# Performance work log

Measured on AMD Instinct MI355X. Metric: run time of the kernel, lower is better.

## Reference

```python
import jax, jax.numpy as jnp
import numpy as np

STRIDE = 16
PRE_K = 600
POST_K = 100
NMS_T = 0.7


def _gen_anchors(base=16.0, ratios=(0.5, 1.0, 2.0), scales=(8.0, 16.0, 32.0)):
    a = []
    for s in scales:
        for r in ratios:
            w = base * s * (r ** 0.5)
            h = base * s / (r ** 0.5)
            a.append([-w / 2, -h / 2, w / 2, h / 2])
    return jnp.asarray(a, jnp.float32)  # [9,4]


def _conv(x, w, b, pad):
    y = jax.lax.conv_general_dilated(x, w, (1, 1), [(pad, pad), (pad, pad)],
                                     dimension_numbers=("NCHW", "OIHW", "NCHW"))
    return y + b[None, :, None, None]


def _decode(deltas, anchors):
    w = anchors[:, 2] - anchors[:, 0]
    h = anchors[:, 3] - anchors[:, 1]
    cx = anchors[:, 0] + 0.5 * w
    cy = anchors[:, 1] + 0.5 * h
    dx, dy, dw, dh = deltas[:, 0], deltas[:, 1], deltas[:, 2], deltas[:, 3]
    pcx = cx + dx * w
    pcy = cy + dy * h
    pw = w * jnp.exp(dw)
    ph = h * jnp.exp(dh)
    return jnp.stack([pcx - 0.5 * pw, pcy - 0.5 * ph,
                      pcx + 0.5 * pw, pcy + 0.5 * ph], axis=-1)


def _nms_keep(boxes, thresh):
    # boxes already sorted by score descending; returns bool keep mask [N]
    x1, y1, x2, y2 = boxes[:, 0], boxes[:, 1], boxes[:, 2], boxes[:, 3]
    area = (x2 - x1) * (y2 - y1)
    xx1 = jnp.maximum(x1[:, None], x1[None, :])
    yy1 = jnp.maximum(y1[:, None], y1[None, :])
    xx2 = jnp.minimum(x2[:, None], x2[None, :])
    yy2 = jnp.minimum(y2[:, None], y2[None, :])
    inter = jnp.maximum(xx2 - xx1, 0.0) * jnp.maximum(yy2 - yy1, 0.0)
    iou = inter / (area[:, None] + area[None, :] - inter)
    n = boxes.shape[0]
    idx = jnp.arange(n)

    def body(i, keep):
        suppress = keep[i] & (iou[i] > thresh) & (idx > i)
        return keep & ~suppress

    return jax.lax.fori_loop(0, n, body, jnp.ones((n,), bool))


def setup_inputs() -> dict:
    key = jax.random.key(0)
    ks = jax.random.split(key, 7)
    C_in, C_mid, A = 256, 256, 9
    feats = jax.random.normal(ks[0], (4, C_in, 128, 128), jnp.float32)
    conv_w = jax.random.normal(ks[1], (C_mid, C_in, 3, 3), jnp.float32) * 0.02
    conv_b = jnp.zeros((C_mid,), jnp.float32)
    cls_w = jax.random.normal(ks[2], (A, C_mid, 1, 1), jnp.float32) * 0.05
    cls_b = jnp.zeros((A,), jnp.float32)
    bbox_w = jax.random.normal(ks[3], (A * 4, C_mid, 1, 1), jnp.float32) * 0.02
    bbox_b = jnp.zeros((A * 4,), jnp.float32)
    return {"features": feats, "conv_w": conv_w, "conv_b": conv_b,
            "cls_w": cls_w, "cls_b": cls_b, "bbox_w": bbox_w, "bbox_b": bbox_b,
            "image_h": 2048, "image_w": 2048}


def reference(features, conv_w, conv_b, cls_w, cls_b, bbox_w, bbox_b, image_h, image_w):
    B, _, H, W = features.shape
    A = cls_w.shape[0]
    t = jax.nn.relu(_conv(features, conv_w, conv_b, 1))
    logits = _conv(t, cls_w, cls_b, 0)        # [B,A,H,W]
    bbox_deltas = _conv(t, bbox_w, bbox_b, 0)  # [B,4A,H,W]

    anchors = _gen_anchors()
    sx = jnp.arange(W, dtype=jnp.float32) * STRIDE
    sy = jnp.arange(H, dtype=jnp.float32) * STRIDE
    gy, gx = jnp.meshgrid(sy, sx, indexing="ij")
    shifts = jnp.stack([gx, gy, gx, gy], axis=2).reshape(-1, 4)  # [HW,4]
    anchors_all = (anchors[None, :, :] + shifts[:, None, :]).reshape(-1, 4)  # [HW*A,4]

    scores = jnp.transpose(logits, (0, 2, 3, 1)).reshape(B, -1)          # [B,HWA]
    deltas = jnp.transpose(bbox_deltas, (0, 2, 3, 1)).reshape(B, -1, 4)  # [B,HWA,4]

    img_w = jnp.float32(image_w)
    img_h = jnp.float32(image_h)

    def per_image(s, d):
        p = _decode(d, anchors_all)
        p = jnp.stack([jnp.clip(p[:, 0], 0.0, img_w),
                       jnp.clip(p[:, 1], 0.0, img_h),
                       jnp.clip(p[:, 2], 0.0, img_w),
                       jnp.clip(p[:, 3], 0.0, img_h)], axis=-1)
        _, topi = jax.lax.top_k(s, PRE_K)
        p = p[topi]                                # [PRE_K,4] sorted by score
        keep = _nms_keep(p, NMS_T)
        order = jnp.argsort(jnp.where(keep, 0, 1), stable=True)  # kept first, score order
        sel = order[:POST_K]
        valid = keep[sel]
        return p[sel] * valid[:, None].astype(p.dtype)  # zero-pad suppressed slots

    return jax.vmap(per_image)(scores, deltas)  # [B,POST_K,4]
```

## Files before the change

### kernel.cpp

```cpp
#include <hip/hip_runtime.h>
#include <cstdint>
#include <cstddef>

#define BB 4
#define CIN 256
#define HH 128
#define WW 128
#define NANCH (HH*WW*9)
#define PRE_K 600
#define POST_K 100
#define NMS_T 0.7f
#define CAND_CAP 2048

typedef _Float16 f16x8 __attribute__((ext_vector_type(8)));
typedef float    f32x4 __attribute__((ext_vector_type(4)));

#define WS_SCORES 0
#define WS_DELTAS (BB*NANCH)
#define WS_WHI    (WS_DELTAS + BB*NANCH*4)
#define WS_WLO    (WS_WHI + 9*256*128)
#define WS_HIST   (WS_WLO + 9*256*128)
#define WS_CCNT   (WS_HIST + 8192)
#define WS_CAND   (WS_CCNT + 16)
#define WS_PHI    (WS_CAND + 16384)
#define WS_PLANE_F 8388608
#define WS_PLO    (WS_PHI + WS_PLANE_F)
#define WS_ZERO   (WS_PLO + WS_PLANE_F)
#define WS_TOTAL_FULL (WS_ZERO + 16)
#define WS_TOTAL_MIN  WS_PHI

__device__ inline unsigned score_key(float f) {
    unsigned u = __float_as_uint(f);
    return (u & 0x80000000u) ? ~u : (u | 0x80000000u);
}

__global__ __launch_bounds__(256)
void prep_all(const float* __restrict__ feat, const float* __restrict__ convw,
              _Float16* __restrict__ pHi, _Float16* __restrict__ pLo,
              _Float16* __restrict__ whi, _Float16* __restrict__ wlo,
              float* __restrict__ zeroPg, unsigned* __restrict__ ghist,
              int prepBlocks)
{
    const int blk = blockIdx.x;
    if (blk < prepBlocks) {
        const int id = blk * 256 + threadIdx.x;
        if (blk == 0 && threadIdx.x < 16) zeroPg[threadIdx.x] = 0.f;
        const int gx = id & 127;
        const int gy = (id >> 7) & 127;
        const int ck = (id >> 14) & 7;
        const int b  = id >> 17;
        const int g  = (((gx + 1) >> 1) & 1) | (((gy + 1) & 1) << 1);
        const float* fb = feat + ((size_t)(b*256 + ck*32) << 14) + (gy << 7) + gx;
        f16x8 gh[4], gl[4];
        #pragma unroll
        for (int icg = 0; icg < 4; ++icg)
            #pragma unroll
            for (int k = 0; k < 8; ++k) {
                const float v = fb[(size_t)(icg*8 + k) << 14] * 16.f;
                const _Float16 h = (_Float16)v;
                gh[icg][k] = h;
                gl[icg][k] = (_Float16)(v - (float)h);
            }
        char* Hc = (char*)pHi + (size_t)id * 64;
        char* Lc = (char*)pLo + (size_t)id * 64;
        #pragma unroll
        for (int icg = 0; icg < 4; ++icg) {
            const int p = icg ^ g;
            *(f16x8*)(Hc + p*16) = gh[icg];
            *(f16x8*)(Lc + p*16) = gl[icg];
        }
    } else if (blk < prepBlocks + 256) {
        const int g = (blk - prepBlocks) * 256 + threadIdx.x;
        if (g >= 65536) return;
        const int oc = g >> 8, ic = g & 255;
        const int chunk = ic >> 5, icl = ic & 31;
        #pragma unroll
        for (int t = 0; t < 9; ++t) {
            const float v = convw[(size_t)g*9 + t] * 64.f;
            const _Float16 h = (_Float16)v;
            const _Float16 lo = (_Float16)(v - (float)h);
            const size_t o = (size_t)((t*8 + chunk)*256 + oc)*32 + icl;
            whi[o] = h;
            wlo[o] = lo;
        }
    } else {
        const int id = (blk - prepBlocks - 256) * 256 + threadIdx.x;
        if (id < 8208) ghist[id] = 0u;
    }
}

__global__ __launch_bounds__(512, 2)
void conv_mfma(const float* __restrict__ feat, const float* __restrict__ convb,
               const _Float16* __restrict__ whi, const _Float16* __restrict__ wlo,
               const float* __restrict__ clsw, const float* __restrict__ bboxw,
               const float* __restrict__ clsb, const float* __restrict__ bboxb,
               const _Float16* __restrict__ pHi, const _Float16* __restrict__ pLo,
               const float* __restrict__ zeroPg, unsigned* __restrict__ ghist,
               float* __restrict__ scores, float* __restrict__ deltas)
{
    __shared__ __align__(16) unsigned char smem[87040];
    float* sBias = (float*)(smem + 86016);

    const int bid = blockIdx.x;
    const int b  = bid >> 6;
    const int ty = (bid >> 3) & 7;
    const int tx = bid & 7;
    const int h0 = ty*16, c0 = tx*16;
    const int tid = threadIdx.x;
    const int w   = tid >> 6;
    const int wm  = w >> 1;
    const int wph = w & 1;
    const int l  = tid & 63;
    const int q  = l >> 4;
    const int c  = l & 15;

    const float* featb = feat + (size_t)b*CIN*HH*WW;
    const int wOff = (wm*64 + c)*32 + q*8;

    if (tid < 256) sBias[tid] = convb[tid] * 1024.f;

    int sdesc[3];
    #pragma unroll
    for (int it = 0; it < 3; ++it) {
        const int e = it*512 + tid;
        if (e < 1344) {
            const int Yl = e / 72, rem = e - Yl*72;
            const int Xl = rem >> 2, p = rem & 3;
            const int gy = h0 - 1 + Yl, gx = c0 - 1 + Xl;
            sdesc[it] = (((unsigned)gy < 128u) && ((unsigned)gx < 128u))
                        ? ((((gy << 7) + gx) << 6) + (p << 4)) : -1;
        } else sdesc[it] = -2;
    }

    auto stage = [&](int ck, int buf) {
        unsigned char* hb = smem + buf*21504;
        unsigned char* lb = smem + 43008 + buf*21504;
        if (pHi) {
            const size_t pb = ((size_t)(b*8 + ck)) << 20;
            #pragma unroll
            for (int pl = 0; pl < 2; ++pl) {
                const char* Ps = (const char*)(pl ? pLo : pHi) + pb;
                unsigned char* Pd = pl ? lb : hb;
                #pragma unroll
                for (int it = 0; it < 3; ++it) {
                    if (sdesc[it] != -2) {
                        const char* src = (sdesc[it] >= 0) ? Ps + sdesc[it]
                                                           : (const char*)zeroPg;
                        __builtin_amdgcn_global_load_lds(
                            (const __attribute__((address_space(1))) void*)src,
                            (__attribute__((address_space(3))) void*)(Pd + it*8192 + tid*16),
                            16, 0, 0);
                    }
                }
            }
        } else {
            const int ic0s = ck*32;
            for (int e = tid; e < 1296; e += 512) {
                const int icg = e / 324, s = e - icg*324;
                const int Y = s / 18, X = s - Y*18;
                const int gy = h0 - 1 + Y, gx = c0 - 1 + X;
                const int g = ((X >> 1) & 1) | ((Y & 1) << 1);
                const bool inb = ((unsigned)gy < 128u) && ((unsigned)gx < 128u);
                f16x8 hv, lv;
                #pragma unroll
                for (int k = 0; k < 8; ++k) {
                    float v = 0.f;
                    if (inb) v = featb[((size_t)(ic0s + icg*8 + k)*HH + gy)*WW + gx];
                    v *= 16.f;
                    const _Float16 h = (_Float16)v;
                    hv[k] = h;
                    lv[k] = (_Float16)(v - (float)h);
                }
                const int base = s*64 + ((icg ^ g) << 4);
                *(f16x8*)(hb + base) = hv;
                *(f16x8*)(lb + base) = lv;
            }
        }
    };

    stage(0, 0);
    __syncthreads();

    f32x4 acc[4][8];
    #pragma unroll
    for (int mf = 0; mf < 4; ++mf) {
        const f32x4 bv = *(const f32x4*)(sBias + (wm*64 + mf*16 + 4*q));
        #pragma unroll
        for (int nf = 0; nf < 8; ++nf) acc[mf][nf] = bv;
    }

    for (int chunk = 0; chunk < 8; ++chunk) {
        const int cur = chunk & 1;
        if (chunk + 1 < 8) stage(chunk + 1, cur ^ 1);
        const unsigned char* hb = smem + cur*21504;
        const unsigned char* lb = smem + 43008 + cur*21504;

        #pragma unroll 3
        for (int t = 0; t < 9; ++t) {
            const int ky = t / 3, kx = t - ky*3;
            const _Float16* pWh = whi + (size_t)(t*8 + chunk)*8192 + wOff;
            const _Float16* pWl = wlo + (size_t)(t*8 + chunk)*8192 + wOff;
            f16x8 ah[4], al[4];
            #pragma unroll
            for (int mf = 0; mf < 4; ++mf) {
                ah[mf] = *(const f16x8*)(const void*)(pWh + mf*512);
                al[mf] = *(const f16x8*)(const void*)(pWl + mf*512);
            }
            #pragma unroll
            for (int nfh = 0; nfh < 2; ++nfh) {
                f16x8 bh[4], bl[4];
                #pragma unroll
                for (int j = 0; j < 4; ++j) {
                    const int nf = nfh*4 + j;
                    const int Y = wph*8 + (nf >> 1)*2 + (c >> 3) + ky;
                    const int X = (nf & 1)*8 + (c & 7) + kx;
                    const int g = ((X >> 1) & 1) | ((Y & 1) << 1);
                    const int addr = (Y*18 + X)*64 + ((q ^ g) << 4);
                    bh[j] = *(const f16x8*)(hb + addr);
                    bl[j] = *(const f16x8*)(lb + addr);
                }
                #pragma unroll
                for (int mf = 0; mf < 4; ++mf)
                    #pragma unroll
                    for (int j = 0; j < 4; ++j) {
                        acc[mf][nfh*4+j] = __builtin_amdgcn_mfma_f32_16x16x32_f16(ah[mf], bh[j], acc[mf][nfh*4+j], 0, 0, 0);
                        acc[mf][nfh*4+j] = __builtin_amdgcn_mfma_f32_16x16x32_f16(ah[mf], bl[j], acc[mf][nfh*4+j], 0, 0, 0);
                        acc[mf][nfh*4+j] = __builtin_amdgcn_mfma_f32_16x16x32_f16(al[mf], bh[j], acc[mf][nfh*4+j], 0, 0, 0);
                    }
            }
        }
        __syncthreads();
    }

    #pragma unroll
    for (int mf = 0; mf < 4; ++mf)
        #pragma unroll
        for (int nf = 0; nf < 8; ++nf)
            #pragma unroll
            for (int r = 0; r < 4; ++r)
                acc[mf][nf][r] = fmaxf(acc[mf][nf][r], 0.f) * 0.0009765625f;

    float*    sW15  = (float*)smem;
    float*    sPart = (float*)(smem + 15360);
    unsigned* sHist = (unsigned*)(smem + 76800);

    for (int e = tid; e < 2048; e += 512) sHist[e] = 0u;

    for (int g = 0; g < 3; ++g) {
        __syncthreads();
        for (int e = tid; e < 3840; e += 512) {
            const int chl = e >> 8, o = e & 255;
            const int ch = g*15 + chl;
            sW15[e] = (ch < 9) ? clsw[ch*256 + o] : bboxw[(ch - 9)*256 + o];
        }
        __syncthreads();
        for (int chl = 0; chl < 15; ++chl) {
            f32x4 wv[4];
            #pragma unroll
            for (int mf = 0; mf < 4; ++mf)
                wv[mf] = *(const f32x4*)(sW15 + chl*256 + wm*64 + mf*16 + 4*q);
            float p[8];
            #pragma unroll
            for (int nf = 0; nf < 8; ++nf) {
                float s = 0.f;
                #pragma unroll
                for (int mf = 0; mf < 4; ++mf)
                    #pragma unroll
                    for (int r = 0; r < 4; ++r)
                        s += wv[mf][r] * acc[mf][nf][r];
                s += __shfl_xor(s, 16, 64);
                s += __shfl_xor(s, 32, 64);
                p[nf] = s;
            }
            const float v0 = (q == 0) ? p[0] : (q == 1) ? p[1] : (q == 2) ? p[2] : p[3];
            const float v1 = (q == 0) ? p[4] : (q == 1) ? p[5] : (q == 2) ? p[6] : p[7];
            sPart[(w*15 + chl)*128 + q*16 + c]      = v0;
            sPart[(w*15 + chl)*128 + 64 + q*16 + c] = v1;
        }
        __syncthreads();
        for (int e = tid; e < 3840; e += 512) {
            const int chl = e >> 8, pxg = e & 255;
            const int ph = pxg >> 7, pxl = pxg & 127;
            float s = 0.f;
            #pragma unroll
            for (int wmq = 0; wmq < 4; ++wmq)
                s += sPart[((wmq*2 + ph)*15 + chl)*128 + pxl];
            const int ch = g*15 + chl;
            s += (ch < 9) ? clsb[ch] : bboxb[ch - 9];
            const int nf = pxl >> 4, cc2 = pxl & 15;
            const int Y = ph*8 + (nf >> 1)*2 + (cc2 >> 3);
            const int X = (nf & 1)*8 + (cc2 & 7);
            const int gy = h0 + Y, gx = c0 + X;
            const int n4 = gy*WW + gx;
            if (ch < 9) {
                scores[(size_t)b*NANCH + n4*9 + ch] = s;
                atomicAdd(&sHist[score_key(s) >> 21], 1u);
            } else {
                const int cc = ch - 9;
                deltas[((size_t)b*NANCH + n4*9 + (cc >> 2))*4 + (cc & 3)] = s;
            }
        }
    }
    for (int e = tid; e < 2048; e += 512) {
        const unsigned cv = sHist[e];
        if (cv) atomicAdd(&ghist[b*2048 + e], cv);
    }
}

__device__ inline void find_thresh(const unsigned* hist, int NB, unsigned target, unsigned* shv)
{
    const int tid = threadIdx.x;
    if (tid < 64) {
        const int gsz = NB >> 5;
        unsigned gsum = 0;
        if (tid < 32)
            for (int k = 0; k < gsz; ++k)
                gsum += hist[tid*gsz + ((k + tid) & (gsz-1))];
        unsigned suf = gsum;
        #pragma unroll
        for (int d = 1; d < 32; d <<= 1) {
            const unsigned t = __shfl_down(suf, d, 64);
            if (tid + d < 32) suf += t;
        }
        const unsigned long long m = __ballot(tid < 32 && suf >= target);
        const int G = 63 - __clzll(m);
        unsigned caboveG = 0;
        { const unsigned t = __shfl(suf, G+1, 64); if (G < 31) caboveG = t; }
        unsigned h = 0;
        if (tid < gsz) h = hist[G*gsz + tid];
        unsigned wsuf = h;
        #pragma unroll
        for (int d = 1; d < 64; d <<= 1) {
            const unsigned t = __shfl_down(wsuf, d, 64);
            if (tid + d < gsz) wsuf += t;
        }
        const unsigned long long m2 = __ballot(tid < gsz && (caboveG + wsuf) >= target);
        const int L = 63 - __clzll(m2);
        if (tid == L) { shv[0] = (unsigned)(G*gsz + L); shv[1] = caboveG + wsuf - h; }
    }
}

__global__ __launch_bounds__(256)
void filter_kernel(const float* __restrict__ scores, const unsigned* __restrict__ ghist,
                   unsigned* __restrict__ ccnt, unsigned long long* __restrict__ cand)
{
    __shared__ unsigned h[2048];
    __shared__ unsigned shv[8];
    const int blk = blockIdx.x;
    const int b = blk >> 6, s = blk & 63;
    const int tid = threadIdx.x;
    const unsigned* hb = ghist + b*2048;
    for (int e = tid; e < 2048; e += 256) h[e] = hb[e];
    __syncthreads();
    find_thresh(h, 2048, PRE_K, shv);
    __syncthreads();
    const unsigned T1 = shv[0];
    const unsigned C  = shv[1] + h[T1];
    const float* si = scores + (size_t)b*NANCH + s*2304;
    if (C <= (unsigned)CAND_CAP) {
        #pragma unroll
        for (int k = 0; k < 9; ++k) {
            const int i = tid + k*256;
            const unsigned u = score_key(si[i]);
            if ((u >> 21) >= T1) {
                const unsigned p = atomicAdd(&ccnt[b], 1u);
                cand[(size_t)b*CAND_CAP + p] =
                    ((unsigned long long)(~u) << 32) | (unsigned)(s*2304 + i);
            }
        }
    } else if (s == 0 && tid == 0) {
        ccnt[b] = 0x7FFFFFFFu;
    }
}

__device__ inline unsigned long long shfl_u64(unsigned long long v, int src) {
    const int lo = __shfl((int)(v & 0xffffffffull), src, 64);
    const int hi = __shfl((int)(v >> 32), src, 64);
    return ((unsigned long long)(unsigned)hi << 32) | (unsigned)lo;
}

__global__ __launch_bounds__(1024)
void post_kernel(const float* __restrict__ scores, const float* __restrict__ deltas,
                 const unsigned* __restrict__ ccnt, const unsigned long long* __restrict__ cand,
                 const int* __restrict__ imh, const int* __restrict__ imw,
                 float* __restrict__ out)
{
    __shared__ unsigned hist[2048];
    __shared__ unsigned long long arr[1024];
    __shared__ unsigned tiebuf[1024];
    __shared__ unsigned shv[8];
    __shared__ unsigned long long arr2[CAND_CAP];
    __shared__ float bx[PRE_K][4];
    __shared__ unsigned long long mrow[PRE_K][10];
    __shared__ unsigned long long keepw[10];
    __shared__ unsigned wpfx[11];
    __shared__ int sel[POST_K];
    const int b = blockIdx.x, tid = threadIdx.x;
    const float* si = scores + (size_t)b*NANCH;

    const unsigned n = ccnt[b];
    const bool fast = (n <= (unsigned)CAND_CAP);
    if (fast) {
        for (int e = tid; e < CAND_CAP; e += 1024)
            arr2[e] = (e < (int)n) ? cand[(size_t)b*CAND_CAP + e] : ~0ull;
        for (unsigned k = 2; k <= (unsigned)CAND_CAP; k <<= 1)
            for (unsigned j = k >> 1; j > 0; j >>= 1) {
                __syncthreads();
                #pragma unroll
                for (int hh = 0; hh < 2; ++hh) {
                    const unsigned i = (unsigned)tid + hh*1024, ixj = i ^ j;
                    if (ixj > i) {
                        const unsigned long long a = arr2[i], c2 = arr2[ixj];
                        if ((a > c2) == ((i & k) == 0)) { arr2[i] = c2; arr2[ixj] = a; }
                    }
                }
            }
        __syncthreads();
    } else {
        for (int i = tid; i < 2048; i += 1024) hist[i] = 0;
        __syncthreads();
        for (int i = tid; i < NANCH; i += 1024)
            atomicAdd(&hist[score_key(si[i]) >> 21], 1u);
        __syncthreads();
        find_thresh(hist, 2048, PRE_K, shv);
        __syncthreads();
        const unsigned T1 = shv[0], gtA = shv[1];
        __syncthreads();

        for (int i = tid; i < 2048; i += 1024) hist[i] = 0;
        __syncthreads();
        for (int i = tid; i < NANCH; i += 1024) {
            const unsigned u = score_key(si[i]);
            if ((u >> 21) == T1) atomicAdd(&hist[(u >> 10) & 0x7FFu], 1u);
        }
        __syncthreads();
        find_thresh(hist, 2048, PRE_K - gtA, shv);
        __syncthreads();
        const unsigned T2 = shv[0], gtB = shv[1];
        const unsigned top22 = (T1 << 11) | T2;
        __syncthreads();

        for (int i = tid; i < 1024; i += 1024) hist[i] = 0;
        __syncthreads();
        for (int i = tid; i < NANCH; i += 1024) {
            const unsigned u = score_key(si[i]);
            if ((u >> 10) == top22) atomicAdd(&hist[u & 0x3FFu], 1u);
        }
        __syncthreads();
        find_thresh(hist, 1024, PRE_K - gtA - gtB, shv);
        if (tid == 0) { shv[4] = 0; shv[5] = 0; }
        __syncthreads();
        const unsigned u_thr = (top22 << 10) | shv[0];
        const unsigned n_greater = gtA + gtB + shv[1];
        __syncthreads();

        for (int i = tid; i < NANCH; i += 1024) {
            const unsigned u = score_key(si[i]);
            if (u > u_thr) {
                const unsigned p = atomicAdd(&shv[4], 1u);
                arr[p] = ((unsigned long long)(~u) << 32) | (unsigned)i;
            } else if (u == u_thr) {
                const unsigned p = atomicAdd(&shv[5], 1u);
                if (p < 1024u) tiebuf[p] = (unsigned)i;
            }
        }
        __syncthreads();
        const unsigned cnt_tie = (shv[5] > 1024u) ? 1024u : shv[5];
        if ((unsigned)tid >= cnt_tie) tiebuf[tid] = 0xFFFFFFFFu;

        for (unsigned k = 2; k <= 1024; k <<= 1)
            for (unsigned j = k >> 1; j > 0; j >>= 1) {
                __syncthreads();
                const unsigned i = (unsigned)tid, ixj = i ^ j;
                if (ixj > i) {
                    const unsigned a = tiebuf[i], cc = tiebuf[ixj];
                    if ((a > cc) == ((i & k) == 0)) { tiebuf[i] = cc; tiebuf[ixj] = a; }
                }
            }
        __syncthreads();
        const unsigned ties_needed = PRE_K - n_greater;
        if ((unsigned)tid < ties_needed)
            arr[n_greater + tid] = ((unsigned long long)(~u_thr) << 32) | tiebuf[tid];
        if (tid >= PRE_K) arr[tid] = ~0ull;

        for (unsigned k = 2; k <= 1024; k <<= 1)
            for (unsigned j = k >> 1; j > 0; j >>= 1) {
                __syncthreads();
                const unsigned i = (unsigned)tid, ixj = i ^ j;
                if (ixj > i) {
                    const unsigned long long a = arr[i], cc = arr[ixj];
                    if ((a > cc) == ((i & k) == 0)) { arr[i] = cc; arr[ixj] = a; }
                }
            }
        __syncthreads();
        if (tid < 1024) arr2[tid] = arr[tid];
        __syncthreads();
    }

    if (tid < PRE_K) {
        const unsigned idx = (unsigned)arr2[tid];
        const int a   = (int)(idx % 9u);
        const int n4  = (int)(idx / 9u);
        const int hh_ = n4 >> 7;
        const int ww_ = n4 & 127;
        const int si_ = a / 3, ri = a % 3;
        const double sq = (ri == 0) ? 0.70710678118654752440 : ((ri == 1) ? 1.0 : 1.41421356237309504880);
        const double sc = (si_ == 0) ? 8.0 : ((si_ == 1) ? 16.0 : 32.0);
        const float half_w = (float)(16.0 * sc * sq * 0.5);
        const float half_h = (float)(16.0 * sc / sq * 0.5);
        const float shx = 16.f * (float)ww_;
        const float shy = 16.f * (float)hh_;
        const float x1a = shx - half_w, x2a = shx + half_w;
        const float y1a = shy - half_h, y2a = shy + half_h;
        const float aw = x2a - x1a, ah = y2a - y1a;
        const float acx = x1a + 0.5f*aw, acy = y1a + 0.5f*ah;
        const float* d = deltas + ((size_t)b*NANCH + idx) * 4;
        const float dx = d[0], dy = d[1], dw = d[2], dh = d[3];
        const float pcx = acx + dx*aw;
        const float pcy = acy + dy*ah;
        const float pw  = aw * expf(dw);
        const float ph  = ah * expf(dh);
        const float fw = (float)imw[0], fh = (float)imh[0];
        bx[tid][0] = fminf(fmaxf(pcx - 0.5f*pw, 0.f), fw);
        bx[tid][1] = fminf(fmaxf(pcy - 0.5f*ph, 0.f), fh);
        bx[tid][2] = fminf(fmaxf(pcx + 0.5f*pw, 0.f), fw);
        bx[tid][3] = fminf(fmaxf(pcy + 0.5f*ph, 0.f), fh);
    }
    __syncthreads();

    for (int item = tid; item < PRE_K*10; item += 1024) {
        const int i  = item / 10;
        const int wj = item - i*10;
        unsigned long long m = 0ull;
        const int jbase = wj * 64;
        if (jbase + 63 > i) {
            const float xi1 = bx[i][0], yi1 = bx[i][1], xi2 = bx[i][2], yi2 = bx[i][3];
            const float ai = (xi2 - xi1) * (yi2 - yi1);
            for (int bit = 0; bit < 64; ++bit) {
                const int j = jbase + bit;
                if (j < PRE_K && j > i) {
                    const float xx1 = fmaxf(xi1, bx[j][0]);
                    const float yy1 = fmaxf(yi1, bx[j][1]);
                    const float xx2 = fminf(xi2, bx[j][2]);
                    const float yy2 = fminf(yi2, bx[j][3]);
                    const float inter = fmaxf(xx2 - xx1, 0.f) * fmaxf(yy2 - yy1, 0.f);
                    const float aj = (bx[j][2] - bx[j][0]) * (bx[j][3] - bx[j][1]);
                    const float iou = inter / (ai + aj - inter);
                    if (iou > NMS_T) m |= (1ull << bit);
                }
            }
        }
        mrow[i][wj] = m;
    }
    __syncthreads();

    if (tid < 64) {
        const int lane = tid;
        unsigned long long kwv;
        if (lane < 9)       kwv = ~0ull;
        else if (lane == 9) kwv = (1ull << (PRE_K - 576)) - 1;
        else                kwv = 0ull;
        for (int w = 0; w < 10; ++w) {
            const int base = w*64;
            const int nb = (w == 9) ? (PRE_K - 576) : 64;
            if (lane == w) {
                for (int bit = 0; bit < nb; ++bit) {
                    const unsigned long long mm = mrow[base + bit][w];
                    if ((kwv >> bit) & 1ull) kwv &= ~mm;
                }
            }
            const unsigned long long fw = shfl_u64(kwv, w);
            if (lane > w && lane < 10) {
                for (int bit = 0; bit < nb; ++bit) {
                    const unsigned long long mm = mrow[base + bit][lane];
                    if ((fw >> bit) & 1ull) kwv &= ~mm;
                }
            }
        }
        if (lane < 10) keepw[lane] = kwv;
    }
    __syncthreads();
    if (tid == 0) {
        unsigned ccount = 0;
        #pragma unroll
        for (int w = 0; w < 10; ++w) { wpfx[w] = ccount; ccount += (unsigned)__popcll(keepw[w]); }
        wpfx[10] = ccount;
    }
    if (tid < POST_K) sel[tid] = -1;
    __syncthreads();
    if (tid < PRE_K) {
        const int w = tid >> 6, bit = tid & 63;
        const unsigned long long kw = keepw[w];
        if ((kw >> bit) & 1ull) {
            const unsigned rank = wpfx[w] + (unsigned)__popcll(kw & ((1ull << bit) - 1ull));
            if (rank < POST_K) sel[rank] = tid;
        }
    }
    __syncthreads();
    if (tid < POST_K) {
        const int s_ = sel[tid];
        float o0 = 0.f, o1 = 0.f, o2 = 0.f, o3 = 0.f;
        if (s_ >= 0) { o0 = bx[s_][0]; o1 = bx[s_][1]; o2 = bx[s_][2]; o3 = bx[s_][3]; }
        float* o = out + (size_t)b*POST_K*4 + tid*4;
        o[0] = o0; o[1] = o1; o[2] = o2; o[3] = o3;
    }
}

extern "C" void kernel_launch(void* const* d_in, const int* in_sizes, int n_in,
                              void* d_out, int out_size, void* d_ws, size_t ws_size,
                              hipStream_t stream) {
    const float* feat  = (const float*)d_in[0];
    const float* convw = (const float*)d_in[1];
    const float* convb = (const float*)d_in[2];
    const float* clsw  = (const float*)d_in[3];
    const float* clsb  = (const float*)d_in[4];
    const float* bboxw = (const float*)d_in[5];
    const float* bboxb = (const float*)d_in[6];
    const int*   imh   = (const int*)d_in[7];
    const int*   imw   = (const int*)d_in[8];

    if (ws_size < (size_t)WS_TOTAL_MIN * sizeof(float)) return;
    const bool use_prep = ws_size >= (size_t)WS_TOTAL_FULL * sizeof(float);

    float*    scores = (float*)d_ws + WS_SCORES;
    float*    deltas = (float*)d_ws + WS_DELTAS;
    _Float16* whi    = (_Float16*)((float*)d_ws + WS_WHI);
    _Float16* wlo    = (_Float16*)((float*)d_ws + WS_WLO);
    unsigned* ghist  = (unsigned*)((float*)d_ws + WS_HIST);
    unsigned* ccnt   = (unsigned*)((float*)d_ws + WS_CCNT);
    unsigned long long* cand = (unsigned long long*)((float*)d_ws + WS_CAND);
    _Float16* pHi    = use_prep ? (_Float16*)((float*)d_ws + WS_PHI) : nullptr;
    _Float16* pLo    = use_prep ? (_Float16*)((float*)d_ws + WS_PLO) : nullptr;
    float*    zeroPg = use_prep ? ((float*)d_ws + WS_ZERO) : nullptr;
    float*    outp   = (float*)d_out;

    const int prepBlocks = use_prep ? 2048 : 0;
    prep_all<<<dim3(prepBlocks + 256 + 33), dim3(256), 0, stream>>>(
        feat, convw, pHi, pLo, whi, wlo, zeroPg, ghist, prepBlocks);
    conv_mfma<<<dim3(256), dim3(512), 0, stream>>>(feat, convb, whi, wlo, clsw, bboxw,
                                                   clsb, bboxb, pHi, pLo, zeroPg, ghist,
                                                   scores, deltas);
    filter_kernel<<<dim3(256), dim3(256), 0, stream>>>(scores, ghist, ccnt, cand);
    post_kernel<<<dim3(BB), dim3(1024), 0, stream>>>(scores, deltas, ccnt, cand,
                                                     imh, imw, outp);
}
```

Baseline: 440.2 us.

## Replace bitonic candidate sort with rank-counting placement and aggregate filter atomics

The filter kernel now collects passing candidates in a shared-memory buffer and reserves global space with one atomic per block, instead of one global atomic per candidate. The per-image counter is padded to its own stride, and the candidate capacity grows so more images stay on the fast path. In the post kernel, the 2048-entry bitonic sort is replaced by an O(n²) rank count: each candidate finds its rank and, if it is in the top 600, writes its decoded box straight to that slot. This removes many barrier-separated sort stages, but the quadratic comparison cost grows with the candidate count and shared memory use rises.

```diff
diff --git a/kernel.cpp b/kernel.cpp
--- a/kernel.cpp
+++ b/kernel.cpp
@@ -10,7 +10,8 @@
 #define PRE_K 600
 #define POST_K 100
 #define NMS_T 0.7f
-#define CAND_CAP 2048
+#define CAND_CAP 8192
+#define CCNT_STRIDE 16
 
 typedef _Float16 f16x8 __attribute__((ext_vector_type(8)));
 typedef float    f32x4 __attribute__((ext_vector_type(4)));
@@ -21,8 +22,8 @@
 #define WS_WLO    (WS_WHI + 9*256*128)
 #define WS_HIST   (WS_WLO + 9*256*128)
 #define WS_CCNT   (WS_HIST + 8192)
-#define WS_CAND   (WS_CCNT + 16)
-#define WS_PHI    (WS_CAND + 16384)
+#define WS_CAND   (WS_CCNT + 64)
+#define WS_PHI    (WS_CAND + BB*CAND_CAP*2)
 #define WS_PLANE_F 8388608
 #define WS_PLO    (WS_PHI + WS_PLANE_F)
 #define WS_ZERO   (WS_PLO + WS_PLANE_F)
@@ -32,6 +33,36 @@
 __device__ inline unsigned score_key(float f) {
     unsigned u = __float_as_uint(f);
     return (u & 0x80000000u) ? ~u : (u | 0x80000000u);
+}
+
+__device__ inline void decode_box(unsigned idx, const float* __restrict__ deltas,
+                                  int b, float fw, float fh, float* o4)
+{
+    const int a   = (int)(idx % 9u);
+    const int n4  = (int)(idx / 9u);
+    const int hh_ = n4 >> 7;
+    const int ww_ = n4 & 127;
+    const int si_ = a / 3, ri = a % 3;
+    const double sq = (ri == 0) ? 0.70710678118654752440 : ((ri == 1) ? 1.0 : 1.41421356237309504880);
+    const double sc = (si_ == 0) ? 8.0 : ((si_ == 1) ? 16.0 : 32.0);
+    const float half_w = (float)(16.0 * sc * sq * 0.5);
+    const float half_h = (float)(16.0 * sc / sq * 0.5);
+    const float shx = 16.f * (float)ww_;
+    const float shy = 16.f * (float)hh_;
+    const float x1a = shx - half_w, x2a = shx + half_w;
+    const float y1a = shy - half_h, y2a = shy + half_h;
+    const float aw = x2a - x1a, ah = y2a - y1a;
+    const float acx = x1a + 0.5f*aw, acy = y1a + 0.5f*ah;
+    const float* d = deltas + ((size_t)b*NANCH + idx) * 4;
+    const float dx = d[0], dy = d[1], dw = d[2], dh = d[3];
+    const float pcx = acx + dx*aw;
+    const float pcy = acy + dy*ah;
+    const float pw  = aw * expf(dw);
+    const float ph  = ah * expf(dh);
+    o4[0] = fminf(fmaxf(pcx - 0.5f*pw, 0.f), fw);
+    o4[1] = fminf(fmaxf(pcy - 0.5f*ph, 0.f), fh);
+    o4[2] = fminf(fmaxf(pcx + 0.5f*pw, 0.f), fw);
+    o4[3] = fminf(fmaxf(pcy + 0.5f*ph, 0.f), fh);
 }
 
 __global__ __launch_bounds__(256)
@@ -85,7 +116,7 @@
         }
     } else {
         const int id = (blk - prepBlocks - 256) * 256 + threadIdx.x;
-        if (id < 8208) ghist[id] = 0u;
+        if (id < 8256) ghist[id] = 0u;
     }
 }
 
@@ -346,10 +377,13 @@
 {
     __shared__ unsigned h[2048];
     __shared__ unsigned shv[8];
+    __shared__ unsigned long long lbuf[2304];
+    __shared__ unsigned lcnt, gbase;
     const int blk = blockIdx.x;
     const int b = blk >> 6, s = blk & 63;
     const int tid = threadIdx.x;
     const unsigned* hb = ghist + b*2048;
+    if (tid == 0) lcnt = 0u;
     for (int e = tid; e < 2048; e += 256) h[e] = hb[e];
     __syncthreads();
     find_thresh(h, 2048, PRE_K, shv);
@@ -363,13 +397,18 @@
             const int i = tid + k*256;
             const unsigned u = score_key(si[i]);
             if ((u >> 21) >= T1) {
-                const unsigned p = atomicAdd(&ccnt[b], 1u);
-                cand[(size_t)b*CAND_CAP + p] =
-                    ((unsigned long long)(~u) << 32) | (unsigned)(s*2304 + i);
-            }
-        }
+                const unsigned p = atomicAdd(&lcnt, 1u);
+                lbuf[p] = ((unsigned long long)(~u) << 32) | (unsigned)(s*2304 + i);
+            }
+        }
+        __syncthreads();
+        if (tid == 0) gbase = atomicAdd(&ccnt[b*CCNT_STRIDE], lcnt);
+        __syncthreads();
+        const unsigned nL = lcnt, base = gbase;
+        for (unsigned e = tid; e < nL; e += 256)
+            cand[(size_t)b*CAND_CAP + base + e] = lbuf[e];
     } else if (s == 0 && tid == 0) {
-        ccnt[b] = 0x7FFFFFFFu;
+        ccnt[b*CCNT_STRIDE] = 0x7FFFFFFFu;
     }
 }
 
@@ -385,36 +424,39 @@
                  const int* __restrict__ imh, const int* __restrict__ imw,
                  float* __restrict__ out)
 {
+    __shared__ unsigned long long cnd[CAND_CAP];
+    __shared__ float bx[PRE_K][4];
+    __shared__ unsigned long long mrow[PRE_K][10];
     __shared__ unsigned hist[2048];
     __shared__ unsigned long long arr[1024];
     __shared__ unsigned tiebuf[1024];
     __shared__ unsigned shv[8];
-    __shared__ unsigned long long arr2[CAND_CAP];
-    __shared__ float bx[PRE_K][4];
-    __shared__ unsigned long long mrow[PRE_K][10];
     __shared__ unsigned long long keepw[10];
     __shared__ unsigned wpfx[11];
     __shared__ int sel[POST_K];
     const int b = blockIdx.x, tid = threadIdx.x;
     const float* si = scores + (size_t)b*NANCH;
-
-    const unsigned n = ccnt[b];
+    const float fw = (float)imw[0], fh = (float)imh[0];
+
+    const unsigned n = ccnt[b*CCNT_STRIDE];
     const bool fast = (n <= (unsigned)CAND_CAP);
+
     if (fast) {
-        for (int e = tid; e < CAND_CAP; e += 1024)
-            arr2[e] = (e < (int)n) ? cand[(size_t)b*CAND_CAP + e] : ~0ull;
-        for (unsigned k = 2; k <= (unsigned)CAND_CAP; k <<= 1)
-            for (unsigned j = k >> 1; j > 0; j >>= 1) {
-                __syncthreads();
-                #pragma unroll
-                for (int hh = 0; hh < 2; ++hh) {
-                    const unsigned i = (unsigned)tid + hh*1024, ixj = i ^ j;
-                    if (ixj > i) {
-                        const unsigned long long a = arr2[i], c2 = arr2[ixj];
-                        if ((a > c2) == ((i & k) == 0)) { arr2[i] = c2; arr2[ixj] = a; }
-                    }
-                }
-            }
+        for (int e = tid; e < (int)n; e += 1024)
+            cnd[e] = cand[(size_t)b*CAND_CAP + e];
+        __syncthreads();
+        for (int e = tid; e < (int)n; e += 1024) {
+            const unsigned long long cv = cnd[e];
+            unsigned rank = 0;
+            for (int e2 = 0; e2 < (int)n; ++e2)
+                rank += (cnd[e2] < cv) ? 1u : 0u;
+            if (rank < PRE_K) {
+                float o4[4];
+                decode_box((unsigned)cv, deltas, b, fw, fh, o4);
+                bx[rank][0] = o4[0]; bx[rank][1] = o4[1];
+                bx[rank][2] = o4[2]; bx[rank][3] = o4[3];
+            }
+        }
         __syncthreads();
     } else {
         for (int i = tid; i < 2048; i += 1024) hist[i] = 0;
@@ -493,40 +535,14 @@
                 }
             }
         __syncthreads();
-        if (tid < 1024) arr2[tid] = arr[tid];
-        __syncthreads();
-    }
-
-    if (tid < PRE_K) {
-        const unsigned idx = (unsigned)arr2[tid];
-        const int a   = (int)(idx % 9u);
-        const int n4  = (int)(idx / 9u);
-        const int hh_ = n4 >> 7;
-        const int ww_ = n4 & 127;
-        const int si_ = a / 3, ri = a % 3;
-        const double sq = (ri == 0) ? 0.70710678118654752440 : ((ri == 1) ? 1.0 : 1.41421356237309504880);
-        const double sc = (si_ == 0) ? 8.0 : ((si_ == 1) ? 16.0 : 32.0);
-        const float half_w = (float)(16.0 * sc * sq * 0.5);
-        const float half_h = (float)(16.0 * sc / sq * 0.5);
-        const float shx = 16.f * (float)ww_;
-        const float shy = 16.f * (float)hh_;
-        const float x1a = shx - half_w, x2a = shx + half_w;
-        const float y1a = shy - half_h, y2a = shy + half_h;
-        const float aw = x2a - x1a, ah = y2a - y1a;
-        const float acx = x1a + 0.5f*aw, acy = y1a + 0.5f*ah;
-        const float* d = deltas + ((size_t)b*NANCH + idx) * 4;
-        const float dx = d[0], dy = d[1], dw = d[2], dh = d[3];
-        const float pcx = acx + dx*aw;
-        const float pcy = acy + dy*ah;
-        const float pw  = aw * expf(dw);
-        const float ph  = ah * expf(dh);
-        const float fw = (float)imw[0], fh = (float)imh[0];
-        bx[tid][0] = fminf(fmaxf(pcx - 0.5f*pw, 0.f), fw);
-        bx[tid][1] = fminf(fmaxf(pcy - 0.5f*ph, 0.f), fh);
-        bx[tid][2] = fminf(fmaxf(pcx + 0.5f*pw, 0.f), fw);
-        bx[tid][3] = fminf(fmaxf(pcy + 0.5f*ph, 0.f), fh);
-    }
-    __syncthreads();
+
+        if (tid < PRE_K) {
+            float o4[4];
+            decode_box((unsigned)arr[tid], deltas, b, fw, fh, o4);
+            bx[tid][0] = o4[0]; bx[tid][1] = o4[1]; bx[tid][2] = o4[2]; bx[tid][3] = o4[3];
+        }
+        __syncthreads();
+    }
 
     for (int item = tid; item < PRE_K*10; item += 1024) {
         const int i  = item / 10;
@@ -569,11 +585,11 @@
                     if ((kwv >> bit) & 1ull) kwv &= ~mm;
                 }
             }
-            const unsigned long long fw = shfl_u64(kwv, w);
+            const unsigned long long fw2 = shfl_u64(kwv, w);
             if (lane > w && lane < 10) {
                 for (int bit = 0; bit < nb; ++bit) {
                     const unsigned long long mm = mrow[base + bit][lane];
-                    if ((fw >> bit) & 1ull) kwv &= ~mm;
+                    if ((fw2 >> bit) & 1ull) kwv &= ~mm;
                 }
             }
         }
```

Result: faster. 426.9 us (-3.0%).
